# Performance work log

Measured on AMD Instinct MI355X. Metric: run time of the kernel, lower is better.

Reference implementation:

```python
import jax, jax.numpy as jnp
import numpy as np

N_NODES = 50000
N_EDGES = 800000
IN_DIM = 128
HID = 128
N_LAYERS = 3
N_CLASSES = 6
NUM_GRAPHS = 64
BN_EPS = 1e-5


def setup_inputs() -> dict:
    key = jax.random.key(0)
    ks = jax.random.split(key, 12)
    x = jax.random.normal(ks[0], (N_NODES, IN_DIM), dtype=jnp.float32)
    edge_index = jax.random.randint(ks[1], (2, N_EDGES), 0, N_NODES, dtype=jnp.int32)
    batch = jnp.sort(jax.random.randint(ks[2], (N_NODES,), 0, NUM_GRAPHS, dtype=jnp.int32))
    s = 1.0 / np.sqrt(HID)
    # stacked per-layer params (all layers are [HID, HID] since IN_DIM == HID)
    Wl = jax.random.uniform(ks[3], (N_LAYERS, HID, HID), jnp.float32, -s, s)  # lin_l (neighbor agg), has bias
    bl = jax.random.uniform(ks[4], (N_LAYERS, HID), jnp.float32, -s, s)
    Wr = jax.random.uniform(ks[5], (N_LAYERS, HID, HID), jnp.float32, -s, s)  # lin_r (root), no bias
    gamma = jnp.ones((N_LAYERS, HID), jnp.float32)
    beta = jnp.zeros((N_LAYERS, HID), jnp.float32)
    W1 = jax.random.uniform(ks[6], (HID // 2, HID), jnp.float32, -s, s)
    b1 = jax.random.uniform(ks[7], (HID // 2,), jnp.float32, -s, s)
    s2 = 1.0 / np.sqrt(HID // 2)
    W2 = jax.random.uniform(ks[8], (N_CLASSES, HID // 2), jnp.float32, -s2, s2)
    b2 = jax.random.uniform(ks[9], (N_CLASSES,), jnp.float32, -s2, s2)
    return {"x": x, "edge_index": edge_index, "batch": batch, "Wl": Wl, "bl": bl,
            "Wr": Wr, "gamma": gamma, "beta": beta, "W1": W1, "b1": b1, "W2": W2, "b2": b2}


def reference(x, edge_index, batch, Wl, bl, Wr, gamma, beta, W1, b1, W2, b2):
    src, dst = edge_index[0], edge_index[1]
    n = x.shape[0]
    # in-degree (for mean aggregation), computed once; clamp to avoid div-by-zero
    deg = jax.ops.segment_sum(jnp.ones((src.shape[0],), x.dtype), dst, num_segments=n)
    deg = jnp.maximum(deg, 1.0)[:, None]
    for l in range(N_LAYERS):
        # SAGEConv: mean-aggregate neighbor features, then lin_l(agg) + lin_r(x)
        agg = jax.ops.segment_sum(x[src], dst, num_segments=n) / deg  # [N, HID]
        h = agg @ Wl[l].T + bl[l] + x @ Wr[l].T
        # BatchNorm1d (training-mode batch statistics over nodes)
        mu = h.mean(axis=0)
        var = h.var(axis=0)
        h = (h - mu) * jax.lax.rsqrt(var + BN_EPS) * gamma[l] + beta[l]
        x = jax.nn.relu(h)  # dropout omitted (eval semantics / deterministic baseline)
    # global_mean_pool over graph ids
    pooled = jax.ops.segment_sum(x, batch, num_segments=NUM_GRAPHS)
    cnt = jax.ops.segment_sum(jnp.ones((n,), x.dtype), batch, num_segments=NUM_GRAPHS)
    pooled = pooled / jnp.maximum(cnt, 1.0)[:, None]
    # MLP head
    h = jax.nn.relu(pooled @ W1.T + b1)
    return h @ W2.T + b2
```

## Files before the change

kernel.cpp:

```cpp
#include <hip/hip_runtime.h>

#define N_NODES 50000
#define N_EDGES 800000
#define DIM 128
#define NLAYERS 3
#define NCLASSES 6
#define NGRAPHS 64
#define BN_EPS 1e-5f

#define SCAN_BLK 256
#define SCAN_NB ((N_NODES + SCAN_BLK - 1) / SCAN_BLK)

#define POOL_CHUNKS 8
#define NPART 16

#define FILL_GRPS 8
#define FILL_BPG 128
#define NODES_PER_GRP ((N_NODES + FILL_GRPS - 1) / FILL_GRPS)

typedef unsigned short ushort_t;
typedef unsigned int uint_t;
using bf16x8 = __attribute__((ext_vector_type(8))) short;
using f32x4 = __attribute__((ext_vector_type(4))) float;

__device__ __forceinline__ float bf2f(ushort_t b) {
  return __uint_as_float(((uint_t)b) << 16);
}
__device__ __forceinline__ ushort_t f2bf(float f) {
  uint_t u = __float_as_uint(f);
  u += 0x7fffu + ((u >> 16) & 1u);
  return (ushort_t)(u >> 16);
}


__global__ void k_count(const int* __restrict__ dst, int* __restrict__ cnt) {
  int e = blockIdx.x * blockDim.x + threadIdx.x;
  if (e < N_EDGES) atomicAdd(&cnt[dst[e]], 1);
}

__global__ void k_scan_a(const int* __restrict__ cnt, int* __restrict__ incl,
                         int* __restrict__ bsum) {
  __shared__ int s[SCAN_BLK];
  int i = blockIdx.x * SCAN_BLK + threadIdx.x;
  int v = (i < N_NODES) ? cnt[i] : 0;
  s[threadIdx.x] = v;
  __syncthreads();
  for (int off = 1; off < SCAN_BLK; off <<= 1) {
    int t = (threadIdx.x >= off) ? s[threadIdx.x - off] : 0;
    __syncthreads();
    s[threadIdx.x] += t;
    __syncthreads();
  }
  if (i < N_NODES) incl[i] = s[threadIdx.x];
  if (threadIdx.x == SCAN_BLK - 1) bsum[blockIdx.x] = s[SCAN_BLK - 1];
}

__global__ void k_scan_b(const int* __restrict__ bsum, int* __restrict__ boff) {
  __shared__ int s[SCAN_BLK];
  int t = threadIdx.x;
  int v = (t < SCAN_NB) ? bsum[t] : 0;
  s[t] = v;
  __syncthreads();
  for (int off = 1; off < SCAN_BLK; off <<= 1) {
    int u = (t >= off) ? s[t - off] : 0;
    __syncthreads();
    s[t] += u;
    __syncthreads();
  }
  boff[t] = s[t] - v;
}

__global__ void k_scan_c(const int* __restrict__ cnt, const int* __restrict__ incl,
                         const int* __restrict__ boff, int* __restrict__ row_ptr,
                         int* __restrict__ cursor, float* __restrict__ degf) {
  int i = blockIdx.x * SCAN_BLK + threadIdx.x;
  if (i < N_NODES) {
    int ex = incl[i] - cnt[i] + boff[blockIdx.x];
    row_ptr[i] = ex;
    cursor[i] = ex;
    degf[i] = (float)max(cnt[i], 1);
  }
  if (i == 0) row_ptr[N_NODES] = N_EDGES;
}

__global__ void k_fill2(const int* __restrict__ src, const int* __restrict__ dst,
                        int* __restrict__ cursor, int* __restrict__ col) {
  int grp = blockIdx.x & (FILL_GRPS - 1);
  int blk = blockIdx.x >> 3;
  int lo = grp * NODES_PER_GRP;
  int hi = min(lo + NODES_PER_GRP, N_NODES);
  int per = (N_EDGES + FILL_BPG - 1) / FILL_BPG;
  int es = blk * per, ee = min(es + per, N_EDGES);
  for (int e = es + (int)threadIdx.x; e < ee; e += (int)blockDim.x) {
    int d = dst[e];
    if (d >= lo && d < hi) {
      int pos = atomicAdd(&cursor[d], 1);
      col[pos] = src[e];
    }
  }
}

__global__ void k_wt2(const float* __restrict__ Wl, const float* __restrict__ Wr,
                      ushort_t* __restrict__ W2) {
  int i = blockIdx.x * blockDim.x + threadIdx.x;
  if (i >= NLAYERS * 8 * 4 * 128) return;
  int c = i & 127;
  int q = (i >> 7) & 3;
  int ks = (i >> 9) & 7;
  int l = i >> 12;
  int kbase = ks * 32 + q * 8;
  size_t obase = (size_t)l * 65536 + ks * 8192 + q * 1024 + c * 8;
#pragma unroll
  for (int kk = 0; kk < 8; ++kk) {
    int k = kbase + kk;
    float w = (k < DIM) ? Wl[(size_t)l * DIM * DIM + c * DIM + k]
                        : Wr[(size_t)l * DIM * DIM + c * DIM + (k - DIM)];
    ushort_t hi = f2bf(w);
    float lo = w - bf2f(hi);
    W2[obase + kk] = hi;
    W2[obase + 4096 + kk] = f2bf(lo);
  }
}

__global__ void k_tobf16(const float* __restrict__ x, ushort_t* __restrict__ xb) {
  int i4 = blockIdx.x * blockDim.x + threadIdx.x;
  if (i4 >= N_NODES * DIM / 4) return;
  float4 v = ((const float4*)x)[i4];
  ushort4 o;
  o.x = f2bf(v.x);
  o.y = f2bf(v.y);
  o.z = f2bf(v.z);
  o.w = f2bf(v.w);
  ((ushort4*)xb)[i4] = o;
}


__global__ void k_gather4(const ushort_t* __restrict__ xb, const int* __restrict__ row_ptr,
                          const int* __restrict__ col, const float* __restrict__ degf,
                          ushort_t* __restrict__ aggb) {
  int wid = threadIdx.x >> 6, lane = threadIdx.x & 63;
  int n = blockIdx.x * 4 + wid;
  if (n >= N_NODES) return;
  int beg = row_ptr[n], end = row_ptr[n + 1];
  int sub = lane >> 4;
  int c16 = lane & 15;
  const uint4* x4 = (const uint4*)xb;
  float a[8] = {0.f, 0.f, 0.f, 0.f, 0.f, 0.f, 0.f, 0.f};
  int p = beg + sub;
  for (; p + 12 < end; p += 16) {
    int c[4];
#pragma unroll
    for (int u = 0; u < 4; ++u) c[u] = col[p + 4 * u];
    uint4 v[4];
#pragma unroll
    for (int u = 0; u < 4; ++u) v[u] = x4[(size_t)c[u] * 16 + c16];
#pragma unroll
    for (int u = 0; u < 4; ++u) {
      a[0] += bf2f((ushort_t)(v[u].x & 0xffffu));
      a[1] += bf2f((ushort_t)(v[u].x >> 16));
      a[2] += bf2f((ushort_t)(v[u].y & 0xffffu));
      a[3] += bf2f((ushort_t)(v[u].y >> 16));
      a[4] += bf2f((ushort_t)(v[u].z & 0xffffu));
      a[5] += bf2f((ushort_t)(v[u].z >> 16));
      a[6] += bf2f((ushort_t)(v[u].w & 0xffffu));
      a[7] += bf2f((ushort_t)(v[u].w >> 16));
    }
  }
  for (; p < end; p += 4) {
    uint4 v = x4[(size_t)col[p] * 16 + c16];
    a[0] += bf2f((ushort_t)(v.x & 0xffffu));
    a[1] += bf2f((ushort_t)(v.x >> 16));
    a[2] += bf2f((ushort_t)(v.y & 0xffffu));
    a[3] += bf2f((ushort_t)(v.y >> 16));
    a[4] += bf2f((ushort_t)(v.z & 0xffffu));
    a[5] += bf2f((ushort_t)(v.z >> 16));
    a[6] += bf2f((ushort_t)(v.w & 0xffffu));
    a[7] += bf2f((ushort_t)(v.w >> 16));
  }
#pragma unroll
  for (int u = 0; u < 8; ++u) {
    a[u] += __shfl_xor(a[u], 16);
    a[u] += __shfl_xor(a[u], 32);
  }
  if (sub == 0) {
    float inv = 1.0f / degf[n];
    uint4 o;
    o.x = (uint_t)f2bf(a[0] * inv) | ((uint_t)f2bf(a[1] * inv) << 16);
    o.y = (uint_t)f2bf(a[2] * inv) | ((uint_t)f2bf(a[3] * inv) << 16);
    o.z = (uint_t)f2bf(a[4] * inv) | ((uint_t)f2bf(a[5] * inv) << 16);
    o.w = (uint_t)f2bf(a[6] * inv) | ((uint_t)f2bf(a[7] * inv) << 16);
    ((uint4*)aggb)[(size_t)n * 16 + c16] = o;
  }
}

__global__ __launch_bounds__(256) void k_mfma(
    const ushort_t* __restrict__ aggb, const ushort_t* __restrict__ xb,
    const ushort_t* __restrict__ W2l, const float* __restrict__ bl,
    float* __restrict__ h, float* __restrict__ sums_part) {
  __shared__ ushort_t Bs[8192];
  __shared__ float Es[4][16][65];
  __shared__ float lsums[256];

  int tid = threadIdx.x;
  int wave = tid >> 6, lane = tid & 63;
  int rw = blockIdx.x * 64 + wave * 16;
  int lr = lane & 15;
  int q = lane >> 4;
  int rowA = rw + lr;
  if (rowA > N_NODES - 1) rowA = N_NODES - 1;

  lsums[tid] = 0.f;

  f32x4 acc[8];
#pragma unroll
  for (int c = 0; c < 8; ++c) acc[c] = (f32x4){0.f, 0.f, 0.f, 0.f};

#pragma unroll 1
  for (int ks = 0; ks < 8; ++ks) {
    const uint4* wsrc = (const uint4*)(W2l + (size_t)ks * 8192);
#pragma unroll
    for (int it = 0; it < 4; ++it) {
      int idx = it * 256 + tid;
      ((uint4*)Bs)[idx] = wsrc[idx];
    }
    __syncthreads();
    const ushort_t* Asrc = (ks < 4) ? aggb : xb;
    int koff = (ks & 3) * 32 + q * 8;
    bf16x8 af = *(const bf16x8*)(Asrc + (size_t)rowA * DIM + koff);
#pragma unroll
    for (int cf = 0; cf < 8; ++cf) {
      int ci = cf * 16 + lr;
      bf16x8 bh = *(const bf16x8*)(Bs + (q * 128 + ci) * 8);
      bf16x8 bo = *(const bf16x8*)(Bs + 4096 + (q * 128 + ci) * 8);
      acc[cf] = __builtin_amdgcn_mfma_f32_16x16x32_bf16(af, bh, acc[cf], 0, 0, 0);
      acc[cf] = __builtin_amdgcn_mfma_f32_16x16x32_bf16(af, bo, acc[cf], 0, 0, 0);
    }
    __syncthreads();
  }

  float ts[2][4] = {{0.f, 0.f, 0.f, 0.f}, {0.f, 0.f, 0.f, 0.f}};
  float tq[2][4] = {{0.f, 0.f, 0.f, 0.f}, {0.f, 0.f, 0.f, 0.f}};
#pragma unroll
  for (int colhalf = 0; colhalf < 2; ++colhalf) {
#pragma unroll
    for (int cf2 = 0; cf2 < 4; ++cf2) {
      f32x4 a = acc[colhalf * 4 + cf2];
#pragma unroll
      for (int i = 0; i < 4; ++i) Es[wave][q * 4 + i][cf2 * 16 + lr] = a[i];
    }
    __syncthreads();
#pragma unroll
    for (int it = 0; it < 4; ++it) {
      int idx = it * 64 + lane;
      int r = idx >> 4, c4 = idx & 15;
      int n = rw + r;
      if (n < N_NODES) {
        int j = colhalf * 64 + c4 * 4;
        float4 v = *(float4*)&Es[wave][r][c4 * 4];
        v.x += bl[j];
        v.y += bl[j + 1];
        v.z += bl[j + 2];
        v.w += bl[j + 3];
        ts[colhalf][0] += v.x;
        ts[colhalf][1] += v.y;
        ts[colhalf][2] += v.z;
        ts[colhalf][3] += v.w;
        tq[colhalf][0] += v.x * v.x;
        tq[colhalf][1] += v.y * v.y;
        tq[colhalf][2] += v.z * v.z;
        tq[colhalf][3] += v.w * v.w;
        *(float4*)(h + (size_t)n * DIM + j) = v;
      }
    }
    __syncthreads();
  }
  {
    int c4 = lane & 15;
#pragma unroll
    for (int colhalf = 0; colhalf < 2; ++colhalf)
#pragma unroll
      for (int u = 0; u < 4; ++u) {
        int j = colhalf * 64 + c4 * 4 + u;
        atomicAdd(&lsums[j], ts[colhalf][u]);
        atomicAdd(&lsums[128 + j], tq[colhalf][u]);
      }
  }
  __syncthreads();
  atomicAdd(&sums_part[(blockIdx.x & (NPART - 1)) * 256 + tid], lsums[tid]);
}

__global__ void k_bnfin(const float* __restrict__ sums_part, const float* __restrict__ gamma,
                        const float* __restrict__ beta, float* __restrict__ bnsc) {
  int j = threadIdx.x;
  float s = 0.f, q = 0.f;
  for (int p = 0; p < NPART; ++p) {
    s += sums_part[p * 256 + j];
    q += sums_part[p * 256 + 128 + j];
  }
  float mu = s * (1.0f / N_NODES);
  float var = q * (1.0f / N_NODES) - mu * mu;
  float sc = gamma[j] * rsqrtf(var + BN_EPS);
  bnsc[j] = sc;
  bnsc[128 + j] = beta[j] - mu * sc;
}

__global__ void k_bn_apply(const float* __restrict__ h, const float* __restrict__ bnsc,
                           ushort_t* __restrict__ xb) {
  int i4 = blockIdx.x * blockDim.x + threadIdx.x;
  if (i4 >= N_NODES * DIM / 4) return;
  int j0 = (i4 * 4) & (DIM - 1);
  float4 v = ((const float4*)h)[i4];
  float o[4] = {v.x, v.y, v.z, v.w};
  ushort4 r;
#pragma unroll
  for (int u = 0; u < 4; ++u) {
    int j = j0 + u;
    o[u] = fmaxf(fmaf(o[u], bnsc[j], bnsc[128 + j]), 0.f);
  }
  r.x = f2bf(o[0]);
  r.y = f2bf(o[1]);
  r.z = f2bf(o[2]);
  r.w = f2bf(o[3]);
  ((ushort4*)xb)[i4] = r;
}


__global__ void k_gbounds(const int* __restrict__ batch, int* __restrict__ gstart) {
  int t = threadIdx.x;
  if (t > NGRAPHS) return;
  if (t == NGRAPHS) {
    gstart[NGRAPHS] = N_NODES;
    return;
  }
  int lo = 0, hi = N_NODES;
  while (lo < hi) {
    int mid = (lo + hi) >> 1;
    if (batch[mid] < t) lo = mid + 1;
    else hi = mid;
  }
  gstart[t] = lo;
}

__global__ void k_pool3(const float* __restrict__ h, const float* __restrict__ bnsc,
                        const int* __restrict__ gstart, float* __restrict__ pooled) {
  int g = blockIdx.x >> 3;
  int ck = blockIdx.x & 7;
  int s = gstart[g], e = gstart[g + 1];
  int len = e - s;
  int per = (len + POOL_CHUNKS - 1) / POOL_CHUNKS;
  int rs = s + ck * per;
  int re = min(rs + per, e);
  int j = threadIdx.x & 127;
  int rg = threadIdx.x >> 7;
  float sc = bnsc[j], sh = bnsc[128 + j];
  float acc = 0.f;
  for (int r = rs + rg; r < re; r += 2)
    acc += fmaxf(fmaf(h[(size_t)r * DIM + j], sc, sh), 0.f);
  __shared__ float sred[2][DIM];
  sred[rg][j] = acc;
  __syncthreads();
  if (rg == 0) atomicAdd(&pooled[g * DIM + j], sred[0][j] + sred[1][j]);
}

__global__ void k_head2(const float* __restrict__ pooled, const int* __restrict__ gstart,
                        const float* __restrict__ W1, const float* __restrict__ b1,
                        const float* __restrict__ W2, const float* __restrict__ b2,
                        float* __restrict__ out) {
  int g = blockIdx.x;
  int tid = threadIdx.x;
  __shared__ float pm[DIM];
  __shared__ float hid[64];
  float inv = 1.0f / fmaxf((float)(gstart[g + 1] - gstart[g]), 1.0f);
  if (tid < DIM) pm[tid] = pooled[g * DIM + tid] * inv;
  __syncthreads();
  {
    int m = tid >> 2, part = tid & 3;
    const float* w = W1 + m * DIM + part * 32;
    const float* pp = pm + part * 32;
    float acc = 0.f;
#pragma unroll
    for (int k = 0; k < 32; ++k) acc += pp[k] * w[k];
    acc += __shfl_down(acc, 1);
    acc += __shfl_down(acc, 2);
    if (part == 0) hid[m] = fmaxf(acc + b1[m], 0.f);
  }
  __syncthreads();
  if (tid < NCLASSES * 8) {
    int c = tid >> 3, pp8 = tid & 7;
    const float* w = W2 + c * 64 + pp8 * 8;
    const float* hh = hid + pp8 * 8;
    float acc = 0.f;
#pragma unroll
    for (int k = 0; k < 8; ++k) acc += hh[k] * w[k];
    acc += __shfl_down(acc, 1);
    acc += __shfl_down(acc, 2);
    acc += __shfl_down(acc, 4);
    if (pp8 == 0) out[g * NCLASSES + c] = acc + b2[c];
  }
}


extern "C" void kernel_launch(void* const* d_in, const int* in_sizes, int n_in,
                              void* d_out, int out_size, void* d_ws, size_t ws_size,
                              hipStream_t stream) {
  const float* x = (const float*)d_in[0];
  const int* edge = (const int*)d_in[1];
  const int* batch = (const int*)d_in[2];
  const float* Wl = (const float*)d_in[3];
  const float* bl = (const float*)d_in[4];
  const float* Wr = (const float*)d_in[5];
  const float* gamma = (const float*)d_in[6];
  const float* beta = (const float*)d_in[7];
  const float* W1 = (const float*)d_in[8];
  const float* b1 = (const float*)d_in[9];
  const float* W2 = (const float*)d_in[10];
  const float* b2 = (const float*)d_in[11];
  float* out = (float*)d_out;

  const int* src = edge;
  const int* dst = edge + N_EDGES;

  char* p = (char*)d_ws;
  auto alloc = [&](size_t bytes) -> void* {
    void* r = (void*)p;
    p += (bytes + 255) & ~(size_t)255;
    return r;
  };
  int* cnt = (int*)alloc(N_NODES * 4);
  int* incl = (int*)alloc(N_NODES * 4);
  int* bsum = (int*)alloc(SCAN_BLK * 4);
  int* boff = (int*)alloc(SCAN_BLK * 4);
  int* row_ptr = (int*)alloc((N_NODES + 1) * 4);
  int* cursor = (int*)alloc(N_NODES * 4);
  int* col = (int*)alloc(N_EDGES * 4);
  float* degf = (float*)alloc(N_NODES * 4);
  ushort_t* W2b = (ushort_t*)alloc((size_t)NLAYERS * 65536 * 2);
  ushort_t* xb0 = (ushort_t*)alloc((size_t)N_NODES * DIM * 2);
  ushort_t* xb_cur = (ushort_t*)alloc((size_t)N_NODES * DIM * 2);
  ushort_t* aggb = (ushort_t*)alloc((size_t)N_NODES * DIM * 2);
  float* hbuf = (float*)alloc((size_t)N_NODES * DIM * 4);
  float* sums_part = (float*)alloc(NPART * 256 * 4);
  float* bnsc = (float*)alloc(2 * DIM * 4);
  float* pooled = (float*)alloc(NGRAPHS * DIM * 4);
  int* gstart = (int*)alloc((NGRAPHS + 1) * 4);

  hipMemsetAsync(cnt, 0, N_NODES * 4, stream);
  k_count<<<(N_EDGES + 255) / 256, 256, 0, stream>>>(dst, cnt);
  k_scan_a<<<SCAN_NB, SCAN_BLK, 0, stream>>>(cnt, incl, bsum);
  k_scan_b<<<1, SCAN_BLK, 0, stream>>>(bsum, boff);
  k_scan_c<<<SCAN_NB, SCAN_BLK, 0, stream>>>(cnt, incl, boff, row_ptr, cursor, degf);
  k_fill2<<<FILL_GRPS * FILL_BPG, 256, 0, stream>>>(src, dst, cursor, col);
  k_wt2<<<(NLAYERS * 8 * 4 * 128 + 255) / 256, 256, 0, stream>>>(Wl, Wr, W2b);
  k_gbounds<<<1, 128, 0, stream>>>(batch, gstart);
  k_tobf16<<<(N_NODES * DIM / 4 + 255) / 256, 256, 0, stream>>>(x, xb0);

  const ushort_t* xin = xb0;
  for (int l = 0; l < NLAYERS; ++l) {
    k_gather4<<<(N_NODES + 3) / 4, 256, 0, stream>>>(xin, row_ptr, col, degf, aggb);
    hipMemsetAsync(sums_part, 0, NPART * 256 * 4, stream);
    k_mfma<<<(N_NODES + 63) / 64, 256, 0, stream>>>(
        aggb, xin, W2b + (size_t)l * 65536, bl + (size_t)l * DIM, hbuf, sums_part);
    k_bnfin<<<1, 128, 0, stream>>>(sums_part, gamma + (size_t)l * DIM,
                                   beta + (size_t)l * DIM, bnsc);
    if (l < NLAYERS - 1) {
      k_bn_apply<<<(N_NODES * DIM / 4 + 255) / 256, 256, 0, stream>>>(hbuf, bnsc, xb_cur);
      xin = xb_cur;
    }
  }

  hipMemsetAsync(pooled, 0, NGRAPHS * DIM * 4, stream);
  k_pool3<<<NGRAPHS * POOL_CHUNKS, 256, 0, stream>>>(hbuf, bnsc, gstart, pooled);
  k_head2<<<NGRAPHS, 256, 0, stream>>>(pooled, gstart, W1, b1, W2, b2, out);
}
```

Before: 358.8 us.

## Read weights directly from global memory and drop block barriers in MFMA kernel

Removes the shared-memory staging of weight tiles, so each wave reads its B fragments straight from global memory (mostly served by L2/L1). This eliminates every __syncthreads in the GEMM loop and epilogue by giving each wave a private epilogue buffer for both column halves. The BN partial sums are now reduced with wave shuffles and atomically added to global memory per wave, replacing the shared-memory atomics. In exchange, global load traffic for weights goes up and there are more global atomics per block.

```diff
diff --git a/kernel.cpp b/kernel.cpp
--- a/kernel.cpp
+++ b/kernel.cpp
@@ -193,13 +193,11 @@
   }
 }
 
-__global__ __launch_bounds__(256) void k_mfma(
+__global__ __launch_bounds__(256) void k_mfma2(
     const ushort_t* __restrict__ aggb, const ushort_t* __restrict__ xb,
     const ushort_t* __restrict__ W2l, const float* __restrict__ bl,
     float* __restrict__ h, float* __restrict__ sums_part) {
-  __shared__ ushort_t Bs[8192];
-  __shared__ float Es[4][16][65];
-  __shared__ float lsums[256];
+  __shared__ float Es[4][2][16][65];
 
   int tid = threadIdx.x;
   int wave = tid >> 6, lane = tid & 63;
@@ -209,46 +207,39 @@
   int rowA = rw + lr;
   if (rowA > N_NODES - 1) rowA = N_NODES - 1;
 
-  lsums[tid] = 0.f;
-
   f32x4 acc[8];
 #pragma unroll
   for (int c = 0; c < 8; ++c) acc[c] = (f32x4){0.f, 0.f, 0.f, 0.f};
 
 #pragma unroll 1
   for (int ks = 0; ks < 8; ++ks) {
-    const uint4* wsrc = (const uint4*)(W2l + (size_t)ks * 8192);
-#pragma unroll
-    for (int it = 0; it < 4; ++it) {
-      int idx = it * 256 + tid;
-      ((uint4*)Bs)[idx] = wsrc[idx];
-    }
-    __syncthreads();
     const ushort_t* Asrc = (ks < 4) ? aggb : xb;
     int koff = (ks & 3) * 32 + q * 8;
     bf16x8 af = *(const bf16x8*)(Asrc + (size_t)rowA * DIM + koff);
+    const ushort_t* wbase = W2l + ks * 8192 + q * 1024;
 #pragma unroll
     for (int cf = 0; cf < 8; ++cf) {
       int ci = cf * 16 + lr;
-      bf16x8 bh = *(const bf16x8*)(Bs + (q * 128 + ci) * 8);
-      bf16x8 bo = *(const bf16x8*)(Bs + 4096 + (q * 128 + ci) * 8);
+      bf16x8 bh = *(const bf16x8*)(wbase + ci * 8);
+      bf16x8 bo = *(const bf16x8*)(wbase + 4096 + ci * 8);
       acc[cf] = __builtin_amdgcn_mfma_f32_16x16x32_bf16(af, bh, acc[cf], 0, 0, 0);
       acc[cf] = __builtin_amdgcn_mfma_f32_16x16x32_bf16(af, bo, acc[cf], 0, 0, 0);
     }
-    __syncthreads();
   }
 
   float ts[2][4] = {{0.f, 0.f, 0.f, 0.f}, {0.f, 0.f, 0.f, 0.f}};
   float tq[2][4] = {{0.f, 0.f, 0.f, 0.f}, {0.f, 0.f, 0.f, 0.f}};
 #pragma unroll
-  for (int colhalf = 0; colhalf < 2; ++colhalf) {
+  for (int colhalf = 0; colhalf < 2; ++colhalf)
 #pragma unroll
     for (int cf2 = 0; cf2 < 4; ++cf2) {
       f32x4 a = acc[colhalf * 4 + cf2];
 #pragma unroll
-      for (int i = 0; i < 4; ++i) Es[wave][q * 4 + i][cf2 * 16 + lr] = a[i];
-    }
-    __syncthreads();
+      for (int i = 0; i < 4; ++i)
+        Es[wave][colhalf][q * 4 + i][cf2 * 16 + lr] = a[i];
+    }
+#pragma unroll
+  for (int colhalf = 0; colhalf < 2; ++colhalf)
 #pragma unroll
     for (int it = 0; it < 4; ++it) {
       int idx = it * 64 + lane;
@@ -256,7 +247,7 @@
       int n = rw + r;
       if (n < N_NODES) {
         int j = colhalf * 64 + c4 * 4;
-        float4 v = *(float4*)&Es[wave][r][c4 * 4];
+        float4 v = *(float4*)&Es[wave][colhalf][r][c4 * 4];
         v.x += bl[j];
         v.y += bl[j + 1];
         v.z += bl[j + 2];
@@ -272,21 +263,22 @@
         *(float4*)(h + (size_t)n * DIM + j) = v;
       }
     }
-    __syncthreads();
-  }
-  {
-    int c4 = lane & 15;
-#pragma unroll
-    for (int colhalf = 0; colhalf < 2; ++colhalf)
-#pragma unroll
-      for (int u = 0; u < 4; ++u) {
-        int j = colhalf * 64 + c4 * 4 + u;
-        atomicAdd(&lsums[j], ts[colhalf][u]);
-        atomicAdd(&lsums[128 + j], tq[colhalf][u]);
+  int part = blockIdx.x & (NPART - 1);
+#pragma unroll
+  for (int ch = 0; ch < 2; ++ch)
+#pragma unroll
+    for (int u = 0; u < 4; ++u) {
+      float s = ts[ch][u], qq = tq[ch][u];
+      s += __shfl_xor(s, 16);
+      s += __shfl_xor(s, 32);
+      qq += __shfl_xor(qq, 16);
+      qq += __shfl_xor(qq, 32);
+      if (lane < 16) {
+        int j = ch * 64 + lane * 4 + u;
+        atomicAdd(&sums_part[part * 256 + j], s);
+        atomicAdd(&sums_part[part * 256 + 128 + j], qq);
       }
-  }
-  __syncthreads();
-  atomicAdd(&sums_part[(blockIdx.x & (NPART - 1)) * 256 + tid], lsums[tid]);
+    }
 }
 
 __global__ void k_bnfin(const float* __restrict__ sums_part, const float* __restrict__ gamma,
@@ -458,7 +450,7 @@
   for (int l = 0; l < NLAYERS; ++l) {
     k_gather4<<<(N_NODES + 3) / 4, 256, 0, stream>>>(xin, row_ptr, col, degf, aggb);
     hipMemsetAsync(sums_part, 0, NPART * 256 * 4, stream);
-    k_mfma<<<(N_NODES + 63) / 64, 256, 0, stream>>>(
+    k_mfma2<<<(N_NODES + 63) / 64, 256, 0, stream>>>(
         aggb, xin, W2b + (size_t)l * 65536, bl + (size_t)l * DIM, hbuf, sums_part);
     k_bnfin<<<1, 128, 0, stream>>>(sums_part, gamma + (size_t)l * DIM,
                                    beta + (size_t)l * DIM, bnsc);
```

After: 379.1 us. 1.06x slower.

## Store pre-BN activations in bf16 and streamline MFMA epilogue reductions

Applied to the files above, without the earlier changes.

The GEMM kernel now writes the pre-BatchNorm activations as bf16 instead of fp32, halving the bytes written there and read back by the BN-apply and pooling kernels, which are updated to read bf16. The weight tile staged in shared memory doubles so there are half as many barrier-separated K steps. The per-column BN statistics are reduced with wave shuffles and per-wave shared slots instead of shared-memory atomics, and redundant barriers in the epilogue are dropped. Statistics are still computed in fp32 before rounding, but the normalized values now come from bf16-rounded h, which adds rounding error.

```diff
diff --git a/kernel.cpp b/kernel.cpp
--- a/kernel.cpp
+++ b/kernel.cpp
@@ -193,13 +193,13 @@
   }
 }
 
-__global__ __launch_bounds__(256) void k_mfma(
+__global__ __launch_bounds__(256) void k_mfma3(
     const ushort_t* __restrict__ aggb, const ushort_t* __restrict__ xb,
     const ushort_t* __restrict__ W2l, const float* __restrict__ bl,
-    float* __restrict__ h, float* __restrict__ sums_part) {
-  __shared__ ushort_t Bs[8192];
+    ushort_t* __restrict__ hb, float* __restrict__ sums_part) {
+  __shared__ ushort_t Bs[16384];
   __shared__ float Es[4][16][65];
-  __shared__ float lsums[256];
+  __shared__ float lsums[4][256];
 
   int tid = threadIdx.x;
   int wave = tid >> 6, lane = tid & 63;
@@ -209,31 +209,32 @@
   int rowA = rw + lr;
   if (rowA > N_NODES - 1) rowA = N_NODES - 1;
 
-  lsums[tid] = 0.f;
-
   f32x4 acc[8];
 #pragma unroll
   for (int c = 0; c < 8; ++c) acc[c] = (f32x4){0.f, 0.f, 0.f, 0.f};
 
 #pragma unroll 1
-  for (int ks = 0; ks < 8; ++ks) {
-    const uint4* wsrc = (const uint4*)(W2l + (size_t)ks * 8192);
-#pragma unroll
-    for (int it = 0; it < 4; ++it) {
-      int idx = it * 256 + tid;
-      ((uint4*)Bs)[idx] = wsrc[idx];
-    }
-    __syncthreads();
-    const ushort_t* Asrc = (ks < 4) ? aggb : xb;
-    int koff = (ks & 3) * 32 + q * 8;
-    bf16x8 af = *(const bf16x8*)(Asrc + (size_t)rowA * DIM + koff);
-#pragma unroll
-    for (int cf = 0; cf < 8; ++cf) {
-      int ci = cf * 16 + lr;
-      bf16x8 bh = *(const bf16x8*)(Bs + (q * 128 + ci) * 8);
-      bf16x8 bo = *(const bf16x8*)(Bs + 4096 + (q * 128 + ci) * 8);
-      acc[cf] = __builtin_amdgcn_mfma_f32_16x16x32_bf16(af, bh, acc[cf], 0, 0, 0);
-      acc[cf] = __builtin_amdgcn_mfma_f32_16x16x32_bf16(af, bo, acc[cf], 0, 0, 0);
+  for (int kp = 0; kp < 4; ++kp) {
+    const uint4* wsrc = (const uint4*)(W2l + (size_t)kp * 16384);
+#pragma unroll
+    for (int it = 0; it < 8; ++it)
+      ((uint4*)Bs)[it * 256 + tid] = wsrc[it * 256 + tid];
+    __syncthreads();
+#pragma unroll
+    for (int kh = 0; kh < 2; ++kh) {
+      int ks = kp * 2 + kh;
+      const ushort_t* Asrc = (ks < 4) ? aggb : xb;
+      int koff = (ks & 3) * 32 + q * 8;
+      bf16x8 af = *(const bf16x8*)(Asrc + (size_t)rowA * DIM + koff);
+      const ushort_t* bbase = Bs + kh * 8192 + q * 1024;
+#pragma unroll
+      for (int cf = 0; cf < 8; ++cf) {
+        int ci = cf * 16 + lr;
+        bf16x8 bh = *(const bf16x8*)(bbase + ci * 8);
+        bf16x8 bo = *(const bf16x8*)(bbase + 4096 + ci * 8);
+        acc[cf] = __builtin_amdgcn_mfma_f32_16x16x32_bf16(af, bh, acc[cf], 0, 0, 0);
+        acc[cf] = __builtin_amdgcn_mfma_f32_16x16x32_bf16(af, bo, acc[cf], 0, 0, 0);
+      }
     }
     __syncthreads();
   }
@@ -248,7 +249,6 @@
 #pragma unroll
       for (int i = 0; i < 4; ++i) Es[wave][q * 4 + i][cf2 * 16 + lr] = a[i];
     }
-    __syncthreads();
 #pragma unroll
     for (int it = 0; it < 4; ++it) {
       int idx = it * 64 + lane;
@@ -269,24 +269,37 @@
         tq[colhalf][1] += v.y * v.y;
         tq[colhalf][2] += v.z * v.z;
         tq[colhalf][3] += v.w * v.w;
-        *(float4*)(h + (size_t)n * DIM + j) = v;
+        ushort4 o;
+        o.x = f2bf(v.x);
+        o.y = f2bf(v.y);
+        o.z = f2bf(v.z);
+        o.w = f2bf(v.w);
+        *(ushort4*)(hb + (size_t)n * DIM + j) = o;
       }
     }
-    __syncthreads();
-  }
-  {
-    int c4 = lane & 15;
-#pragma unroll
-    for (int colhalf = 0; colhalf < 2; ++colhalf)
+  }
+#pragma unroll
+  for (int ch = 0; ch < 2; ++ch)
+#pragma unroll
+    for (int u = 0; u < 4; ++u) {
+      ts[ch][u] += __shfl_xor(ts[ch][u], 16);
+      ts[ch][u] += __shfl_xor(ts[ch][u], 32);
+      tq[ch][u] += __shfl_xor(tq[ch][u], 16);
+      tq[ch][u] += __shfl_xor(tq[ch][u], 32);
+    }
+  if (lane < 16) {
+#pragma unroll
+    for (int ch = 0; ch < 2; ++ch)
 #pragma unroll
       for (int u = 0; u < 4; ++u) {
-        int j = colhalf * 64 + c4 * 4 + u;
-        atomicAdd(&lsums[j], ts[colhalf][u]);
-        atomicAdd(&lsums[128 + j], tq[colhalf][u]);
+        int j = ch * 64 + lr * 4 + u;
+        lsums[wave][j] = ts[ch][u];
+        lsums[wave][128 + j] = tq[ch][u];
       }
   }
   __syncthreads();
-  atomicAdd(&sums_part[(blockIdx.x & (NPART - 1)) * 256 + tid], lsums[tid]);
+  float tot = lsums[0][tid] + lsums[1][tid] + lsums[2][tid] + lsums[3][tid];
+  atomicAdd(&sums_part[(blockIdx.x & (NPART - 1)) * 256 + tid], tot);
 }
 
 __global__ void k_bnfin(const float* __restrict__ sums_part, const float* __restrict__ gamma,
@@ -304,13 +317,13 @@
   bnsc[128 + j] = beta[j] - mu * sc;
 }
 
-__global__ void k_bn_apply(const float* __restrict__ h, const float* __restrict__ bnsc,
-                           ushort_t* __restrict__ xb) {
+__global__ void k_bn_apply2(const ushort_t* __restrict__ hb, const float* __restrict__ bnsc,
+                            ushort_t* __restrict__ xb) {
   int i4 = blockIdx.x * blockDim.x + threadIdx.x;
   if (i4 >= N_NODES * DIM / 4) return;
   int j0 = (i4 * 4) & (DIM - 1);
-  float4 v = ((const float4*)h)[i4];
-  float o[4] = {v.x, v.y, v.z, v.w};
+  ushort4 v = ((const ushort4*)hb)[i4];
+  float o[4] = {bf2f(v.x), bf2f(v.y), bf2f(v.z), bf2f(v.w)};
   ushort4 r;
 #pragma unroll
   for (int u = 0; u < 4; ++u) {
@@ -341,7 +354,7 @@
   gstart[t] = lo;
 }
 
-__global__ void k_pool3(const float* __restrict__ h, const float* __restrict__ bnsc,
+__global__ void k_pool4(const ushort_t* __restrict__ hb, const float* __restrict__ bnsc,
                         const int* __restrict__ gstart, float* __restrict__ pooled) {
   int g = blockIdx.x >> 3;
   int ck = blockIdx.x & 7;
@@ -350,16 +363,26 @@
   int per = (len + POOL_CHUNKS - 1) / POOL_CHUNKS;
   int rs = s + ck * per;
   int re = min(rs + per, e);
-  int j = threadIdx.x & 127;
-  int rg = threadIdx.x >> 7;
-  float sc = bnsc[j], sh = bnsc[128 + j];
-  float acc = 0.f;
-  for (int r = rs + rg; r < re; r += 2)
-    acc += fmaxf(fmaf(h[(size_t)r * DIM + j], sc, sh), 0.f);
-  __shared__ float sred[2][DIM];
-  sred[rg][j] = acc;
-  __syncthreads();
-  if (rg == 0) atomicAdd(&pooled[g * DIM + j], sred[0][j] + sred[1][j]);
+  int j2 = threadIdx.x & 63;
+  int rg = threadIdx.x >> 6;
+  const uint_t* h1 = (const uint_t*)hb;
+  float sc0 = bnsc[2 * j2], sh0 = bnsc[128 + 2 * j2];
+  float sc1 = bnsc[2 * j2 + 1], sh1 = bnsc[128 + 2 * j2 + 1];
+  float ax = 0.f, ay = 0.f;
+  for (int r = rs + rg; r < re; r += 4) {
+    uint_t v = h1[(size_t)r * 64 + j2];
+    ax += fmaxf(fmaf(bf2f((ushort_t)(v & 0xffffu)), sc0, sh0), 0.f);
+    ay += fmaxf(fmaf(bf2f((ushort_t)(v >> 16)), sc1, sh1), 0.f);
+  }
+  __shared__ float sred[4][DIM];
+  sred[rg][2 * j2] = ax;
+  sred[rg][2 * j2 + 1] = ay;
+  __syncthreads();
+  if (rg < 2) {
+    int j = rg * 64 + j2;
+    float v = sred[0][j] + sred[1][j] + sred[2][j] + sred[3][j];
+    atomicAdd(&pooled[g * DIM + j], v);
+  }
 }
 
 __global__ void k_head2(const float* __restrict__ pooled, const int* __restrict__ gstart,
@@ -438,7 +461,7 @@
   ushort_t* xb0 = (ushort_t*)alloc((size_t)N_NODES * DIM * 2);
   ushort_t* xb_cur = (ushort_t*)alloc((size_t)N_NODES * DIM * 2);
   ushort_t* aggb = (ushort_t*)alloc((size_t)N_NODES * DIM * 2);
-  float* hbuf = (float*)alloc((size_t)N_NODES * DIM * 4);
+  ushort_t* hb = (ushort_t*)alloc((size_t)N_NODES * DIM * 2);
   float* sums_part = (float*)alloc(NPART * 256 * 4);
   float* bnsc = (float*)alloc(2 * DIM * 4);
   float* pooled = (float*)alloc(NGRAPHS * DIM * 4);
@@ -458,17 +481,17 @@
   for (int l = 0; l < NLAYERS; ++l) {
     k_gather4<<<(N_NODES + 3) / 4, 256, 0, stream>>>(xin, row_ptr, col, degf, aggb);
     hipMemsetAsync(sums_part, 0, NPART * 256 * 4, stream);
-    k_mfma<<<(N_NODES + 63) / 64, 256, 0, stream>>>(
-        aggb, xin, W2b + (size_t)l * 65536, bl + (size_t)l * DIM, hbuf, sums_part);
+    k_mfma3<<<(N_NODES + 63) / 64, 256, 0, stream>>>(
+        aggb, xin, W2b + (size_t)l * 65536, bl + (size_t)l * DIM, hb, sums_part);
     k_bnfin<<<1, 128, 0, stream>>>(sums_part, gamma + (size_t)l * DIM,
                                    beta + (size_t)l * DIM, bnsc);
     if (l < NLAYERS - 1) {
-      k_bn_apply<<<(N_NODES * DIM / 4 + 255) / 256, 256, 0, stream>>>(hbuf, bnsc, xb_cur);
+      k_bn_apply2<<<(N_NODES * DIM / 4 + 255) / 256, 256, 0, stream>>>(hb, bnsc, xb_cur);
       xin = xb_cur;
     }
   }
 
   hipMemsetAsync(pooled, 0, NGRAPHS * DIM * 4, stream);
-  k_pool3<<<NGRAPHS * POOL_CHUNKS, 256, 0, stream>>>(hbuf, bnsc, gstart, pooled);
+  k_pool4<<<NGRAPHS * POOL_CHUNKS, 256, 0, stream>>>(hb, bnsc, gstart, pooled);
   k_head2<<<NGRAPHS, 256, 0, stream>>>(pooled, gstart, W1, b1, W2, b2, out);
 }
```

After: 305.1 us. -15.0%, faster.
